# Kernel optimization log

Hardware: AMD Instinct MI355X
Metric: run time of the kernel (lower is better)

Reference implementation:

```python
import jax, jax.numpy as jnp
import numpy as np

D_MODEL = 1024
D_KV = 64
N_HEADS = 16
KV_HEADS = 4
G = N_HEADS // KV_HEADS
NUM_BUCKETS = 32
MAX_DISTANCE = 128


def _relative_position_bucket(relative_position, bidirectional=True,
                              num_buckets=NUM_BUCKETS, max_distance=MAX_DISTANCE):
    # Faithful port of T5Attention._relative_position_bucket
    relative_buckets = jnp.zeros_like(relative_position)
    if bidirectional:
        num_buckets //= 2
        relative_buckets = (relative_position > 0).astype(jnp.int32) * num_buckets
        relative_position = jnp.abs(relative_position)
    else:
        relative_position = -jnp.minimum(relative_position, 0)
    max_exact = num_buckets // 2
    is_small = relative_position < max_exact
    rel_if_large = max_exact + (
        jnp.log(relative_position.astype(jnp.float32) / max_exact)
        / np.log(max_distance / max_exact) * (num_buckets - max_exact)
    ).astype(jnp.int32)
    rel_if_large = jnp.minimum(rel_if_large, num_buckets - 1)
    return relative_buckets + jnp.where(is_small, relative_position, rel_if_large)


def setup_inputs() -> dict:
    key = jax.random.key(0)
    ks = jax.random.split(key, 6)
    B, S = 2, 2048
    inner = N_HEADS * D_KV
    sc = 1.0 / np.sqrt(D_MODEL)
    return {
        "hidden_states": jax.random.normal(ks[0], (B, S, D_MODEL), dtype=jnp.float32),
        "Wq": jax.random.normal(ks[1], (D_MODEL, inner), dtype=jnp.float32) * sc,
        "Wk": jax.random.normal(ks[2], (D_MODEL, inner), dtype=jnp.float32) * sc,
        "Wv": jax.random.normal(ks[3], (D_MODEL, inner), dtype=jnp.float32) * sc,
        "Wo": jax.random.normal(ks[4], (inner, D_MODEL), dtype=jnp.float32) * sc,
        "rel_bias": jax.random.normal(ks[5], (NUM_BUCKETS, N_HEADS), dtype=jnp.float32) * 0.1,
    }


def reference(hidden_states, Wq, Wk, Wv, Wo, rel_bias):
    B, S, _ = hidden_states.shape

    def split_heads(x):  # [B,S,inner] -> [B,H,S,Dk]
        return x.reshape(B, S, N_HEADS, D_KV).transpose(0, 2, 1, 3)

    q = split_heads(hidden_states @ Wq)
    k = split_heads(hidden_states @ Wk)
    v = split_heads(hidden_states @ Wv)

    # head index = g * KV_HEADS + h (einops 'b (g h) ...' with h=kv_heads)
    gq = q.reshape(B, G, KV_HEADS, S, D_KV)
    gk = k.reshape(B, G, KV_HEADS, S, D_KV).mean(axis=1)  # [B,Hkv,S,Dk]
    # einsum sums over g (as in torch.einsum 'bghnd,bhsd->bhns'); no 1/sqrt(d) in T5
    scores = jnp.einsum('bghnd,bhsd->bhns', gq, gk)  # [B,Hkv,S,S]

    # T5 relative position bias (bidirectional, encoder)
    ctx = jnp.arange(S)[:, None]
    mem = jnp.arange(S)[None, :]
    buckets = _relative_position_bucket(mem - ctx, bidirectional=True)
    bias = rel_bias[buckets]                # [S,S,H]
    bias = bias.transpose(2, 0, 1)[None]    # [1,H,S,S]
    gbias = bias.reshape(1, G, KV_HEADS, S, S).mean(axis=1)  # [1,Hkv,S,S]

    scores = scores + gbias
    attn = jax.nn.softmax(scores.astype(jnp.float32), axis=-1).astype(scores.dtype)

    # repeat grouped attn weights back to full heads: 'b h n s -> b (g h) n s'
    attn_full = jnp.tile(attn, (1, G, 1, 1))  # [B,H,S,S]
    ctx_out = jnp.einsum('bhns,bhsd->bhnd', attn_full, v)  # [B,H,S,Dk]
    ctx_out = ctx_out.transpose(0, 2, 1, 3).reshape(B, S, N_HEADS * D_KV)
    return ctx_out @ Wo  # [B,S,D_MODEL]
```

## Files before the change

### kernel.cpp

```cpp
#include <hip/hip_runtime.h>
#include <math.h>


typedef __bf16 bf16_t;
typedef bf16_t bf16x8 __attribute__((ext_vector_type(8)));
typedef bf16_t bf16x4 __attribute__((ext_vector_type(4)));
typedef float f32x4 __attribute__((ext_vector_type(4)));

#define MFMA16(a, b, c) __builtin_amdgcn_mfma_f32_16x16x32_bf16(a, b, c, 0, 0, 0)

typedef __attribute__((address_space(1))) void gvoid;
typedef __attribute__((address_space(3))) void svoid;
__device__ __forceinline__ void gld16(const void* g, void* l) {
    __builtin_amdgcn_global_load_lds((gvoid*)g, (svoid*)l, 16, 0, 0);
}

__global__ __launch_bounds__(256) void prep_all(const float* __restrict__ hs,
                                                const float* __restrict__ Wq,
                                                const float* __restrict__ Wk,
                                                const float* __restrict__ Wv,
                                                const float* __restrict__ Wo,
                                                const float* __restrict__ rel_bias,
                                                bf16_t* __restrict__ hs_hi,
                                                bf16_t* __restrict__ hs_lo,
                                                bf16_t* __restrict__ Thi,
                                                bf16_t* __restrict__ Tlo,
                                                bf16_t* __restrict__ WvT,
                                                bf16_t* __restrict__ WoT,
                                                float* __restrict__ btab) {
    __shared__ float sm[2048];
    const int r = blockIdx.x, t = threadIdx.x;
    if (r < 4096) {
        size_t idx = ((size_t)r * 256 + t) * 4;
        float4 v = *(const float4*)(hs + idx);
        bf16x4 h, l;
        h[0] = (bf16_t)v.x; l[0] = (bf16_t)(v.x - (float)h[0]);
        h[1] = (bf16_t)v.y; l[1] = (bf16_t)(v.y - (float)h[1]);
        h[2] = (bf16_t)v.z; l[2] = (bf16_t)(v.z - (float)h[2]);
        h[3] = (bf16_t)v.w; l[3] = (bf16_t)(v.w - (float)h[3]);
        *(bf16x4*)(hs_hi + idx) = h;
        *(bf16x4*)(hs_lo + idx) = l;
    } else if (r < 5120) {
        int k = r - 4096;
        float* rq = sm;
        float* rk = sm + 1024;
#pragma unroll
        for (int j = 0; j < 4; ++j) {
            rq[t + j * 256] = Wq[(size_t)k * 1024 + t + j * 256];
            rk[t + j * 256] = Wk[(size_t)k * 1024 + t + j * 256];
        }
        __syncthreads();
        int h = t >> 6, j2 = t & 63;
        float sq = 0.f, sk = 0.f;
#pragma unroll
        for (int g = 0; g < 4; ++g) {
            sq += rq[(g * 4 + h) * 64 + j2];
            sk += rk[(g * 4 + h) * 64 + j2];
        }
        sk *= 0.25f;
        bf16_t qh = (bf16_t)sq;
        Thi[(size_t)t * 1024 + k] = qh;
        Tlo[(size_t)t * 1024 + k] = (bf16_t)(sq - (float)qh);
        bf16_t kh = (bf16_t)sk;
        Thi[(size_t)(256 + t) * 1024 + k] = kh;
        Tlo[(size_t)(256 + t) * 1024 + k] = (bf16_t)(sk - (float)kh);
    } else if (r < 7168) {
        const float* src = (r < 6144) ? Wv : Wo;
        bf16_t* dst = (r < 6144) ? WvT : WoT;
        int rr = (r < 6144) ? r - 5120 : r - 6144;
        int bx = (rr & 31) * 32, by = (rr >> 5) * 32;
        int tx = t & 31, ty = t >> 5;
        float(*tile)[33] = (float(*)[33])sm;
#pragma unroll
        for (int i = 0; i < 32; i += 8)
            tile[ty + i][tx] = src[(size_t)(by + ty + i) * 1024 + bx + tx];
        __syncthreads();
#pragma unroll
        for (int i = 0; i < 32; i += 8)
            dst[(size_t)(bx + ty + i) * 1024 + by + tx] = (bf16_t)tile[tx][ty + i];
    } else {
        int idx = (r - 7168) * 256 + t;
        if (idx >= 4095) return;
        int delta = idx - 2047;
        int bucket = (delta > 0) ? 16 : 0;
        int arp = delta < 0 ? -delta : delta;
        int rb;
        if (arp < 8) {
            rb = arp;
        } else {
            float tt = (logf((float)arp * 0.125f) / 2.772588722239781f) * 8.0f;
            int ri = 8 + (int)tt;
            rb = ri < 15 ? ri : 15;
        }
        bucket += rb;
#pragma unroll
        for (int h = 0; h < 4; ++h) {
            float s = 0.25f * (rel_bias[bucket * 16 + h] + rel_bias[bucket * 16 + h + 4] +
                               rel_bias[bucket * 16 + h + 8] + rel_bias[bucket * 16 + h + 12]);
            btab[h * 4608 + idx] = s;
        }
    }
}

__global__ __launch_bounds__(256, 1) void proj_qkv(const bf16_t* __restrict__ Ah,
                                                   const bf16_t* __restrict__ Al,
                                                   const bf16_t* __restrict__ Bh,
                                                   const bf16_t* __restrict__ Bl,
                                                   const bf16_t* __restrict__ WvT,
                                                   bf16_t* __restrict__ Qhi,
                                                   bf16_t* __restrict__ Qlo,
                                                   bf16_t* __restrict__ Kbh,
                                                   bf16_t* __restrict__ Kbl,
                                                   bf16_t* __restrict__ Vb) {
    __shared__ bf16_t pool[36864];
    const int K = 1024, nk = 32;
    const int t = threadIdx.x;
    const int w = t >> 6, lane = t & 63;
    const int lr = lane & 15, q = lane >> 4;
    const int l = blockIdx.y * 16 + blockIdx.x;
    const int nl = (l & 7) * 64 + (l >> 3);
    const int bx = nl & 15;
    const int m0 = (nl >> 4) * 128;
    const bool qk = bx < 8;
    const int n0 = qk ? bx * 64 : (bx - 8) * 128;
    const int mw = (w & 1) * 64;
    f32x4 acc[4][4] = {};

    const int rA = t & 127, cA0 = t >> 7, cA1 = 2 + (t >> 7);
    const size_t oA0 = (size_t)(m0 + rA) * K + cA0 * 8;
    const size_t oA1 = (size_t)(m0 + rA) * K + cA1 * 8;
    const int rBq = t & 63, cBq = t >> 6;
    const size_t oBq = (size_t)(n0 + rBq) * K + cBq * 8;
    const size_t oBv0 = (size_t)(n0 + rA) * K + cA0 * 8;
    const size_t oBv1 = (size_t)(n0 + rA) * K + cA1 * 8;

    auto stage = [&](int bf, int kidx) {
        bf16_t* base = &pool[bf * 12288];
        const int k0 = kidx * 32;
        gld16(Ah + oA0 + k0, base + t * 8);
        gld16(Ah + oA1 + k0, base + (256 + t) * 8);
        if (qk) {
            gld16(Al + oA0 + k0, base + 4096 + t * 8);
            gld16(Al + oA1 + k0, base + 4096 + (256 + t) * 8);
            gld16(Bh + oBq + k0, base + 8192 + t * 8);
            gld16(Bl + oBq + k0, base + 10240 + t * 8);
        } else {
            gld16(WvT + oBv0 + k0, base + 4096 + t * 8);
            gld16(WvT + oBv1 + k0, base + 4096 + (256 + t) * 8);
        }
    };

    stage(0, 0);
    stage(1, 1);
    stage(2, 2);
    if (qk)
        asm volatile("s_waitcnt vmcnt(12)" ::: "memory");
    else
        asm volatile("s_waitcnt vmcnt(8)" ::: "memory");
    __builtin_amdgcn_s_barrier();

    int cur = 0;
    for (int it = 0; it < nk; ++it) {
        const bf16_t* base = &pool[cur * 12288];
        if (qk) {
            const int nw = (w >> 1) * 32;
            bf16x8 ah[4], al[4], bh[2], bl[2];
#pragma unroll
            for (int i = 0; i < 4; ++i) {
                int sa = (q * 128 + mw + i * 16 + lr) * 8;
                ah[i] = *(const bf16x8*)&base[sa];
                al[i] = *(const bf16x8*)&base[4096 + sa];
            }
#pragma unroll
            for (int j = 0; j < 2; ++j) {
                int sb = (q * 64 + nw + j * 16 + lr) * 8;
                bh[j] = *(const bf16x8*)&base[8192 + sb];
                bl[j] = *(const bf16x8*)&base[10240 + sb];
            }
            asm volatile("s_waitcnt lgkmcnt(0)" ::: "memory");
            if (it < nk - 2)
                asm volatile("s_waitcnt vmcnt(6)" ::: "memory");
            else
                asm volatile("s_waitcnt vmcnt(0)" ::: "memory");
            __builtin_amdgcn_s_barrier();
            if (it + 3 < nk) stage(cur, it + 3);
#pragma unroll
            for (int i = 0; i < 4; ++i)
#pragma unroll
                for (int j = 0; j < 2; ++j) {
                    acc[i][j] = MFMA16(ah[i], bh[j], acc[i][j]);
                    acc[i][j] = MFMA16(ah[i], bl[j], acc[i][j]);
                    acc[i][j] = MFMA16(al[i], bh[j], acc[i][j]);
                }
        } else {
            const int nw = (w >> 1) * 64;
            bf16x8 af[4], bfv[4];
#pragma unroll
            for (int i = 0; i < 4; ++i)
                af[i] = *(const bf16x8*)&base[(q * 128 + mw + i * 16 + lr) * 8];
#pragma unroll
            for (int j = 0; j < 4; ++j)
                bfv[j] = *(const bf16x8*)&base[4096 + (q * 128 + nw + j * 16 + lr) * 8];
            asm volatile("s_waitcnt lgkmcnt(0)" ::: "memory");
            if (it < nk - 2)
                asm volatile("s_waitcnt vmcnt(4)" ::: "memory");
            else
                asm volatile("s_waitcnt vmcnt(0)" ::: "memory");
            __builtin_amdgcn_s_barrier();
            if (it + 3 < nk) stage(cur, it + 3);
#pragma unroll
            for (int i = 0; i < 4; ++i)
#pragma unroll
                for (int j = 0; j < 4; ++j) acc[i][j] = MFMA16(af[i], bfv[j], acc[i][j]);
        }
        cur = (cur == 2) ? 0 : cur + 1;
    }

    if (qk) {
        const int nwq = (w >> 1) * 32;
#pragma unroll
        for (int i = 0; i < 4; ++i) {
            int row = m0 + mw + i * 16 + q * 4;
#pragma unroll
            for (int j = 0; j < 2; ++j) {
                int col = n0 + nwq + j * 16 + lr;
#pragma unroll
                for (int reg = 0; reg < 4; ++reg) {
                    float x = acc[i][j][reg];
                    int token = row + reg;
                    bf16_t hi = (bf16_t)x;
                    bf16_t lo = (bf16_t)(x - (float)hi);
                    if (col < 256) {
                        size_t o = (size_t)token * 256 + col;
                        Qhi[o] = hi;
                        Qlo[o] = lo;
                    } else {
                        int hc = col - 256;
                        int hh = hc >> 6, d = hc & 63;
                        int b = token >> 11, s = token & 2047;
                        int it2 = s >> 6, sl = s & 63;
                        size_t o = ((size_t)((b * 4 + hh) * 32 + it2)) * 4096 +
                                   (size_t)((d >> 3) * 64 + sl) * 8 + (d & 7);
                        Kbh[o] = hi;
                        Kbl[o] = lo;
                    }
                }
            }
        }
    } else {
        const int nwq = (w >> 1) * 64;
#pragma unroll
        for (int i = 0; i < 4; ++i) {
            int row = m0 + mw + i * 16 + q * 4;
            int b = row >> 11, s = row & 2047;
            int it2 = s >> 6, sc2 = (s >> 3) & 7, si = s & 7;
#pragma unroll
            for (int j = 0; j < 4; ++j) {
                int col = n0 + nwq + j * 16 + lr;
                int hh = (col >> 6) & 3, g = col >> 8, d = col & 63;
                size_t o = ((size_t)((b * 4 + hh) * 32 + it2)) * 16384 +
                           (size_t)(sc2 * 256 + g * 64 + d) * 8 + si;
                bf16x4 pv;
#pragma unroll
                for (int reg = 0; reg < 4; ++reg) pv[reg] = (bf16_t)acc[i][j][reg];
                *(bf16x4*)(Vb + o) = pv;
            }
        }
    }
}

__global__ __launch_bounds__(256, 1) void gemm_out(const bf16_t* __restrict__ A,
                                                   const bf16_t* __restrict__ BT,
                                                   float* __restrict__ C,
                                                   int M, int N, int K) {
    __shared__ bf16_t pool[18432];
    const int t = threadIdx.x;
    const int w = t >> 6, lane = t & 63;
    const int lr = lane & 15, q = lane >> 4;
    const int l = blockIdx.y * 16 + blockIdx.x;
    const int nl = (l & 7) * 64 + (l >> 3);
    const int m0 = (nl >> 4) * 128, n0 = (nl & 15) * 64;
    const int mw = (w & 1) * 64, nw = (w >> 1) * 32;
    f32x4 acc[4][2] = {};
    const int nk = K >> 5;

    const int rA = t & 127, cA0 = t >> 7, cA1 = 2 + (t >> 7);
    const bf16_t* gA0 = A + (size_t)(m0 + rA) * K + cA0 * 8;
    const bf16_t* gA1 = A + (size_t)(m0 + rA) * K + cA1 * 8;
    const bf16_t* gB = BT + (size_t)(n0 + (t & 63)) * K + (t >> 6) * 8;

    auto stage = [&](int bf, int kidx) {
        bf16_t* base = &pool[bf * 6144];
        const int k0 = kidx * 32;
        gld16(gA0 + k0, base + t * 8);
        gld16(gA1 + k0, base + (256 + t) * 8);
        gld16(gB + k0, base + 4096 + t * 8);
    };

    stage(0, 0);
    stage(1, 1);
    stage(2, 2);
    asm volatile("s_waitcnt vmcnt(6)" ::: "memory");
    __builtin_amdgcn_s_barrier();

    int cur = 0;
    for (int it = 0; it < nk; ++it) {
        const bf16_t* base = &pool[cur * 6144];
        bf16x8 af[4], bfv[2];
#pragma unroll
        for (int i = 0; i < 4; ++i)
            af[i] = *(const bf16x8*)&base[(q * 128 + mw + i * 16 + lr) * 8];
#pragma unroll
        for (int j = 0; j < 2; ++j)
            bfv[j] = *(const bf16x8*)&base[4096 + (q * 64 + nw + j * 16 + lr) * 8];
        asm volatile("s_waitcnt lgkmcnt(0)" ::: "memory");
        if (it < nk - 2)
            asm volatile("s_waitcnt vmcnt(3)" ::: "memory");
        else
            asm volatile("s_waitcnt vmcnt(0)" ::: "memory");
        __builtin_amdgcn_s_barrier();
        if (it + 3 < nk) stage(cur, it + 3);
#pragma unroll
        for (int i = 0; i < 4; ++i)
#pragma unroll
            for (int j = 0; j < 2; ++j) acc[i][j] = MFMA16(af[i], bfv[j], acc[i][j]);
        cur = (cur == 2) ? 0 : cur + 1;
    }

#pragma unroll
    for (int i = 0; i < 4; ++i) {
        int row = m0 + mw + i * 16 + q * 4;
#pragma unroll
        for (int j = 0; j < 2; ++j) {
            int col = n0 + nw + j * 16 + lr;
#pragma unroll
            for (int reg = 0; reg < 4; ++reg)
                C[(size_t)(row + reg) * N + col] = acc[i][j][reg];
        }
    }
}

__global__ __launch_bounds__(512, 1) void attn_mfma(const bf16_t* __restrict__ Qhi,
                                                    const bf16_t* __restrict__ Qlo,
                                                    const bf16_t* __restrict__ Kbh,
                                                    const bf16_t* __restrict__ Kbl,
                                                    const bf16_t* __restrict__ Vb,
                                                    const float* __restrict__ btab,
                                                    bf16_t* __restrict__ part0,
                                                    bf16_t* __restrict__ part1,
                                                    float* __restrict__ Sml) {
    __shared__ bf16_t Kh[2][4096], Kl[2][4096], Vsm[16384], Ps[8192];
    const int t = threadIdx.x, w = t >> 6, lane = t & 63;
    const int lr = lane & 15, q = lane >> 4;
    const int bl0 = blockIdx.x;
    const int blk = (bl0 & 7) * 32 + (bl0 >> 3);
    const int half = blk & 1, qt = (blk >> 1) & 15, h = (blk >> 5) & 3, b = blk >> 7;
    const int n0 = qt * 128;
    const int rowbase = n0 + w * 16;
    const int swz = (lr & 7) << 3;
    const int psb = w * 1024 + lr * 64;

    const size_t qrow = (size_t)(b * 2048 + rowbase + lr) * 256 + h * 64;
    bf16x8 aqh[2], aql[2];
#pragma unroll
    for (int kb = 0; kb < 2; ++kb) {
        aqh[kb] = *(const bf16x8*)(Qhi + qrow + kb * 32 + q * 8);
        aql[kb] = *(const bf16x8*)(Qlo + qrow + kb * 32 + q * 8);
    }

    const int tilebase = (b * 4 + h) * 32 + half * 16;
    const bf16_t* gK = Kbh + (size_t)tilebase * 4096;
    const bf16_t* gL = Kbl + (size_t)tilebase * 4096;
    const bf16_t* gV = Vb + (size_t)tilebase * 16384;
    const float* btabh = btab + h * 4608 + 2047;
    const float bpos = btabh[1024];
    const float bneg = btabh[-1024];

    auto stageK = [&](int bf, int it) {
        gld16(gK + (size_t)it * 4096 + t * 8, &Kh[bf][t * 8]);
        gld16(gL + (size_t)it * 4096 + t * 8, &Kl[bf][t * 8]);
    };
    auto stageV = [&](int it) {
        const bf16_t* v0 = gV + (size_t)it * 16384;
#pragma unroll
        for (int j = 0; j < 4; ++j)
            gld16(v0 + (j * 512 + t) * 8, &Vsm[(j * 512 + t) * 8]);
    };

    float m_r = -INFINITY, l_r = 0.f;
    f32x4 O[16] = {};

    stageK(0, 0);
    stageV(0);
    __syncthreads();
    for (int it = 0; it < 16; ++it) {
        const int cur = it & 1;
        if (it + 1 < 16) stageK(cur ^ 1, it + 1);
        const int s0g = half * 1024 + it * 64;

        f32x4 sc[4];
#pragma unroll
        for (int ct = 0; ct < 4; ++ct) {
            f32x4 z = {0.f, 0.f, 0.f, 0.f};
#pragma unroll
            for (int kb = 0; kb < 2; ++kb) {
                int sb = ((kb * 4 + q) * 64 + ct * 16 + lr) * 8;
                bf16x8 bh = *(const bf16x8*)&Kh[cur][sb];
                bf16x8 bl = *(const bf16x8*)&Kl[cur][sb];
                z = MFMA16(bh, aqh[kb], z);
                z = MFMA16(bh, aql[kb], z);
                z = MFMA16(bl, aqh[kb], z);
            }
            sc[ct] = z;
        }
        if (s0g - rowbase >= 143) {
#pragma unroll
            for (int ct = 0; ct < 4; ++ct)
#pragma unroll
                for (int reg = 0; reg < 4; ++reg) sc[ct][reg] += bpos;
        } else if (rowbase - s0g >= 154) {
#pragma unroll
            for (int ct = 0; ct < 4; ++ct)
#pragma unroll
                for (int reg = 0; reg < 4; ++reg) sc[ct][reg] += bneg;
        } else {
            const int dbase = (s0g + q * 4) - (rowbase + lr);
#pragma unroll
            for (int ct = 0; ct < 4; ++ct)
#pragma unroll
                for (int reg = 0; reg < 4; ++reg)
                    sc[ct][reg] += btabh[dbase + ct * 16 + reg];
        }

        float mt = fmaxf(fmaxf(sc[0][0], sc[0][1]), fmaxf(sc[0][2], sc[0][3]));
#pragma unroll
        for (int ct = 1; ct < 4; ++ct)
            mt = fmaxf(mt, fmaxf(fmaxf(sc[ct][0], sc[ct][1]), fmaxf(sc[ct][2], sc[ct][3])));
        mt = fmaxf(mt, __shfl_xor(mt, 16, 64));
        mt = fmaxf(mt, __shfl_xor(mt, 32, 64));

        float mn = fmaxf(m_r, mt);
        const bool noresc = (bool)__all(mn == m_r);
        float al = noresc ? 1.f : __expf(m_r - mn);
        m_r = mn;
        float rs = 0.f;
#pragma unroll
        for (int ct = 0; ct < 4; ++ct) {
            bf16x4 tq;
#pragma unroll
            for (int reg = 0; reg < 4; ++reg) {
                float p = __expf(sc[ct][reg] - mn);
                rs += p;
                tq[reg] = (bf16_t)p;
            }
            *(bf16x4*)&Ps[psb + ((ct * 16 + q * 4) ^ swz)] = tq;
        }
        rs += __shfl_xor(rs, 16, 64);
        rs += __shfl_xor(rs, 32, 64);
        l_r = l_r * al + rs;

        if (!noresc) {
#pragma unroll
            for (int nt = 0; nt < 16; ++nt)
#pragma unroll
                for (int reg = 0; reg < 4; ++reg) O[nt][reg] *= al;
        }

        __syncthreads();

        bf16x8 pf0 = *(const bf16x8*)&Ps[psb + ((q * 8) ^ swz)];
        bf16x8 pf1 = *(const bf16x8*)&Ps[psb + ((32 + q * 8) ^ swz)];

#pragma unroll
        for (int nt = 0; nt < 16; ++nt) {
            f32x4 o = O[nt];
            bf16x8 v0 = *(const bf16x8*)&Vsm[(q * 256 + nt * 16 + lr) * 8];
            o = MFMA16(v0, pf0, o);
            bf16x8 v1 = *(const bf16x8*)&Vsm[((4 + q) * 256 + nt * 16 + lr) * 8];
            o = MFMA16(v1, pf1, o);
            O[nt] = o;
        }
        __syncthreads();
        if (it + 1 < 16) stageV(it + 1);
    }

    bf16_t* P = half ? part1 : part0;
    const float inv = 1.f / l_r;
    const int tokb = b * 2048 + rowbase;
#pragma unroll
    for (int G = 0; G < 4; ++G) {
#pragma unroll
        for (int g4 = 0; g4 < 4; ++g4) {
            int nt = G * 4 + g4;
            bf16x4 tq;
#pragma unroll
            for (int reg = 0; reg < 4; ++reg) tq[reg] = (bf16_t)(O[nt][reg] * inv);
            *(bf16x4*)&Ps[psb + ((g4 * 16 + q * 4) ^ swz)] = tq;
        }
#pragma unroll
        for (int i = 0; i < 2; ++i) {
            int row = i * 8 + (lane >> 3), cv = (lane & 7) * 8;
            bf16x8 fr = *(const bf16x8*)&Ps[w * 1024 + row * 64 + (cv ^ ((row & 7) << 3))];
            *(bf16x8*)(P + (size_t)(tokb + row) * 1024 + (G * 4 + h) * 64 + cv) = fr;
        }
    }
    if (lane < 16)
        Sml[half * 16384 + (size_t)(tokb + lane) * 4 + h] = m_r + logf(l_r);
}

__global__ __launch_bounds__(256) void combine_halves(bf16_t* __restrict__ p0,
                                                      const bf16_t* __restrict__ p1,
                                                      const float* __restrict__ Sml) {
    size_t flat = ((size_t)blockIdx.x * 256 + threadIdx.x) * 8;
    int tok = (int)(flat >> 10), c = (int)(flat & 1023), h = (c >> 6) & 3;
    float s0 = Sml[tok * 4 + h], s1 = Sml[16384 + tok * 4 + h];
    float M = fmaxf(s0, s1);
    float e0 = __expf(s0 - M), e1 = __expf(s1 - M);
    float r = 1.f / (e0 + e1);
    float w0 = e0 * r, w1 = e1 * r;
    bf16x8 a = *(bf16x8*)(p0 + flat);
    bf16x8 bb = *(const bf16x8*)(p1 + flat);
    bf16x8 o;
#pragma unroll
    for (int i = 0; i < 8; ++i) o[i] = (bf16_t)(w0 * (float)a[i] + w1 * (float)bb[i]);
    *(bf16x8*)(p0 + flat) = o;
}

extern "C" void kernel_launch(void* const* d_in, const int* in_sizes, int n_in,
                              void* d_out, int out_size, void* d_ws, size_t ws_size,
                              hipStream_t stream) {
    const float* hs = (const float*)d_in[0];
    const float* Wq = (const float*)d_in[1];
    const float* Wk = (const float*)d_in[2];
    const float* Wv = (const float*)d_in[3];
    const float* Wo = (const float*)d_in[4];
    const float* rb = (const float*)d_in[5];
    float* out = (float*)d_out;

    const size_t MB = 1 << 20;
    const size_t KB = 1 << 10;
    char* ws = (char*)d_ws;
    bf16_t* hs_hi = (bf16_t*)(ws);
    bf16_t* hs_lo = (bf16_t*)(ws + 8 * MB);
    bf16_t* WqkThi = (bf16_t*)(ws + 16 * MB);
    bf16_t* WqkTlo = (bf16_t*)(ws + 17 * MB);
    bf16_t* WvT = (bf16_t*)(ws + 18 * MB);
    bf16_t* WoT = (bf16_t*)(ws + 20 * MB);
    float* btab = (float*)(ws + 22 * MB);
    float* Sml = (float*)(ws + 22 * MB + 128 * KB);
    bf16_t* Qhi = (bf16_t*)(ws + 22 * MB + 256 * KB);
    bf16_t* Qlo = Qhi + (size_t)4096 * 256;
    bf16_t* Kbh = Qlo + (size_t)4096 * 256;
    bf16_t* Kbl = Kbh + (size_t)4096 * 256;
    bf16_t* Vb = Kbl + (size_t)4096 * 256;
    bf16_t* part0 = hs_hi;
    bf16_t* part1 = hs_lo;

    prep_all<<<7184, 256, 0, stream>>>(hs, Wq, Wk, Wv, Wo, rb, hs_hi, hs_lo, WqkThi,
                                       WqkTlo, WvT, WoT, btab);
    proj_qkv<<<dim3(16, 32), 256, 0, stream>>>(hs_hi, hs_lo, WqkThi, WqkTlo, WvT, Qhi,
                                               Qlo, Kbh, Kbl, Vb);
    attn_mfma<<<256, 512, 0, stream>>>(Qhi, Qlo, Kbh, Kbl, Vb, btab, part0, part1, Sml);
    combine_halves<<<2048, 256, 0, stream>>>(part0, part1, Sml);
    gemm_out<<<dim3(16, 32), 256, 0, stream>>>(part0, WoT, out, 4096, 1024, 1024);
}
```

Before: 226.5 us.

## Double-buffer V tiles in attention and batch weight reductions in prep

The attention kernel now double-buffers the V tile alongside K. It prefetches the next iteration's K and V together at the top of the loop, so the V load overlaps the QK and softmax work instead of waiting behind the trailing barrier. It also drops the barrier between writing and reading P, since each wave only touches its own region of P. The prep kernel's Wq/Wk grouped-head reduction now handles 8 k-rows per block and writes them as vectorized 16-byte stores, which cuts that section from 1024 blocks to 128. The cost is twice the LDS for V (about 112 KB total), which rules out a second block per CU. Correctness also now depends on wave-local LDS ordering for P.

```diff
diff --git a/kernel.cpp b/kernel.cpp
--- a/kernel.cpp
+++ b/kernel.cpp
@@ -40,34 +40,38 @@
         h[3] = (bf16_t)v.w; l[3] = (bf16_t)(v.w - (float)h[3]);
         *(bf16x4*)(hs_hi + idx) = h;
         *(bf16x4*)(hs_lo + idx) = l;
-    } else if (r < 5120) {
-        int k = r - 4096;
-        float* rq = sm;
-        float* rk = sm + 1024;
-#pragma unroll
-        for (int j = 0; j < 4; ++j) {
-            rq[t + j * 256] = Wq[(size_t)k * 1024 + t + j * 256];
-            rk[t + j * 256] = Wk[(size_t)k * 1024 + t + j * 256];
-        }
-        __syncthreads();
-        int h = t >> 6, j2 = t & 63;
-        float sq = 0.f, sk = 0.f;
-#pragma unroll
-        for (int g = 0; g < 4; ++g) {
-            sq += rq[(g * 4 + h) * 64 + j2];
-            sk += rk[(g * 4 + h) * 64 + j2];
-        }
-        sk *= 0.25f;
-        bf16_t qh = (bf16_t)sq;
-        Thi[(size_t)t * 1024 + k] = qh;
-        Tlo[(size_t)t * 1024 + k] = (bf16_t)(sq - (float)qh);
-        bf16_t kh = (bf16_t)sk;
-        Thi[(size_t)(256 + t) * 1024 + k] = kh;
-        Tlo[(size_t)(256 + t) * 1024 + k] = (bf16_t)(sk - (float)kh);
-    } else if (r < 7168) {
-        const float* src = (r < 6144) ? Wv : Wo;
-        bf16_t* dst = (r < 6144) ? WvT : WoT;
-        int rr = (r < 6144) ? r - 5120 : r - 6144;
+    } else if (r < 4224) {
+        const int k0 = (r - 4096) * 8;
+        const int h = t >> 6, j2 = t & 63;
+        bf16x8 qh8, ql8, kh8, kl8;
+#pragma unroll
+        for (int kk = 0; kk < 8; ++kk) {
+            const float* wqr = Wq + (size_t)(k0 + kk) * 1024;
+            const float* wkr = Wk + (size_t)(k0 + kk) * 1024;
+            float sq = 0.f, sk = 0.f;
+#pragma unroll
+            for (int g = 0; g < 4; ++g) {
+                int c = (g * 4 + h) * 64 + j2;
+                sq += wqr[c];
+                sk += wkr[c];
+            }
+            sk *= 0.25f;
+            bf16_t qh = (bf16_t)sq;
+            qh8[kk] = qh;
+            ql8[kk] = (bf16_t)(sq - (float)qh);
+            bf16_t kh = (bf16_t)sk;
+            kh8[kk] = kh;
+            kl8[kk] = (bf16_t)(sk - (float)kh);
+        }
+        *(bf16x8*)(Thi + (size_t)t * 1024 + k0) = qh8;
+        *(bf16x8*)(Tlo + (size_t)t * 1024 + k0) = ql8;
+        *(bf16x8*)(Thi + (size_t)(256 + t) * 1024 + k0) = kh8;
+        *(bf16x8*)(Tlo + (size_t)(256 + t) * 1024 + k0) = kl8;
+    } else if (r < 6272) {
+        int rr = r - 4224;
+        const float* src = (rr < 1024) ? Wv : Wo;
+        bf16_t* dst = (rr < 1024) ? WvT : WoT;
+        if (rr >= 1024) rr -= 1024;
         int bx = (rr & 31) * 32, by = (rr >> 5) * 32;
         int tx = t & 31, ty = t >> 5;
         float(*tile)[33] = (float(*)[33])sm;
@@ -79,7 +83,7 @@
         for (int i = 0; i < 32; i += 8)
             dst[(size_t)(bx + ty + i) * 1024 + by + tx] = (bf16_t)tile[tx][ty + i];
     } else {
-        int idx = (r - 7168) * 256 + t;
+        int idx = (r - 6272) * 256 + t;
         if (idx >= 4095) return;
         int delta = idx - 2047;
         int bucket = (delta > 0) ? 16 : 0;
@@ -349,7 +353,7 @@
                                                     bf16_t* __restrict__ part0,
                                                     bf16_t* __restrict__ part1,
                                                     float* __restrict__ Sml) {
-    __shared__ bf16_t Kh[2][4096], Kl[2][4096], Vsm[16384], Ps[8192];
+    __shared__ bf16_t Kh[2][4096], Kl[2][4096], Vsm[2][16384], Ps[8192];
     const int t = threadIdx.x, w = t >> 6, lane = t & 63;
     const int lr = lane & 15, q = lane >> 4;
     const int bl0 = blockIdx.x;
@@ -376,26 +380,23 @@
     const float bpos = btabh[1024];
     const float bneg = btabh[-1024];
 
-    auto stageK = [&](int bf, int it) {
+    auto stage = [&](int bf, int it) {
         gld16(gK + (size_t)it * 4096 + t * 8, &Kh[bf][t * 8]);
         gld16(gL + (size_t)it * 4096 + t * 8, &Kl[bf][t * 8]);
-    };
-    auto stageV = [&](int it) {
         const bf16_t* v0 = gV + (size_t)it * 16384;
 #pragma unroll
         for (int j = 0; j < 4; ++j)
-            gld16(v0 + (j * 512 + t) * 8, &Vsm[(j * 512 + t) * 8]);
+            gld16(v0 + (j * 512 + t) * 8, &Vsm[bf][(j * 512 + t) * 8]);
     };
 
     float m_r = -INFINITY, l_r = 0.f;
     f32x4 O[16] = {};
 
-    stageK(0, 0);
-    stageV(0);
+    stage(0, 0);
     __syncthreads();
     for (int it = 0; it < 16; ++it) {
         const int cur = it & 1;
-        if (it + 1 < 16) stageK(cur ^ 1, it + 1);
+        if (it + 1 < 16) stage(cur ^ 1, it + 1);
         const int s0g = half * 1024 + it * 64;
 
         f32x4 sc[4];
@@ -466,22 +467,19 @@
                 for (int reg = 0; reg < 4; ++reg) O[nt][reg] *= al;
         }
 
-        __syncthreads();
-
         bf16x8 pf0 = *(const bf16x8*)&Ps[psb + ((q * 8) ^ swz)];
         bf16x8 pf1 = *(const bf16x8*)&Ps[psb + ((32 + q * 8) ^ swz)];
 
 #pragma unroll
         for (int nt = 0; nt < 16; ++nt) {
             f32x4 o = O[nt];
-            bf16x8 v0 = *(const bf16x8*)&Vsm[(q * 256 + nt * 16 + lr) * 8];
+            bf16x8 v0 = *(const bf16x8*)&Vsm[cur][(q * 256 + nt * 16 + lr) * 8];
             o = MFMA16(v0, pf0, o);
-            bf16x8 v1 = *(const bf16x8*)&Vsm[((4 + q) * 256 + nt * 16 + lr) * 8];
+            bf16x8 v1 = *(const bf16x8*)&Vsm[cur][((4 + q) * 256 + nt * 16 + lr) * 8];
             o = MFMA16(v1, pf1, o);
             O[nt] = o;
         }
         __syncthreads();
-        if (it + 1 < 16) stageV(it + 1);
     }
 
     bf16_t* P = half ? part1 : part0;
@@ -556,7 +554,7 @@
     bf16_t* part0 = hs_hi;
     bf16_t* part1 = hs_lo;
 
-    prep_all<<<7184, 256, 0, stream>>>(hs, Wq, Wk, Wv, Wo, rb, hs_hi, hs_lo, WqkThi,
+    prep_all<<<6288, 256, 0, stream>>>(hs, Wq, Wk, Wv, Wo, rb, hs_hi, hs_lo, WqkThi,
                                        WqkTlo, WvT, WoT, btab);
     proj_qkv<<<dim3(16, 32), 256, 0, stream>>>(hs_hi, hs_lo, WqkThi, WqkTlo, WvT, Qhi,
                                                Qlo, Kbh, Kbl, Vb);
```

Measured after the change: 222.9 us. Within noise of the previous version (-1.6%).
